# Kernel optimization log

Measured on AMD Instinct MI355X. Metric: run time of the kernel, lower is better.

The kernel has to match this reference:

```python
import jax, jax.numpy as jnp
import numpy as np

N_NODES = 20000  # number of batch nodes (static for segment ops)

def setup_inputs() -> dict:
    key = jax.random.key(0)
    N, E, V, D = N_NODES, 640000, 100000, 64
    ks = jax.random.split(key, 8)
    nodes = jax.random.randint(ks[0], (N,), 0, V)
    neigh_idx = jax.random.randint(ks[1], (E,), 0, V)
    seg_ids = jnp.sort(jax.random.randint(ks[2], (E,), 0, N))  # ragged degrees, sorted by node
    u2e = jax.random.normal(ks[3], (V, D), jnp.float32) * 0.02
    s1 = 1.0 / np.sqrt(2 * D)
    s2 = 1.0 / np.sqrt(D)
    att1_w = jax.random.uniform(ks[4], (2 * D, D), jnp.float32, -s1, s1)
    att1_b = jnp.zeros((D,), jnp.float32)
    att2_w = jax.random.uniform(ks[5], (D, D), jnp.float32, -s2, s2)
    att2_b = jnp.zeros((D,), jnp.float32)
    att3_w = jax.random.uniform(ks[6], (D, 1), jnp.float32, -s2, s2)
    att3_b = jnp.zeros((1,), jnp.float32)
    return dict(nodes=nodes, neigh_idx=neigh_idx, seg_ids=seg_ids, u2e=u2e,
                att1_w=att1_w, att1_b=att1_b, att2_w=att2_w, att2_b=att2_b,
                att3_w=att3_w, att3_b=att3_b)


def reference(nodes, neigh_idx, seg_ids, u2e, att1_w, att1_b, att2_w, att2_b, att3_w, att3_b):
    # Ragged per-node neighbor attention, flattened over all edges.
    e_u = u2e[neigh_idx]              # [E, D] neighbor embeddings
    u_rep = u2e[nodes][seg_ids]       # [E, D] center-node embedding broadcast per edge
    x = jnp.concatenate([e_u, u_rep], axis=1)            # [E, 2D]
    x = jax.nn.relu(x @ att1_w + att1_b)                  # [E, D]
    x = jax.nn.relu(x @ att2_w + att2_b)                  # [E, D]
    logits = (x @ att3_w + att3_b)[:, 0]                  # [E]
    # segment softmax over each node's neighbor set
    m = jax.ops.segment_max(logits, seg_ids, num_segments=N_NODES)
    m = jnp.where(jnp.isfinite(m), m, 0.0)                # guard empty segments
    ex = jnp.exp(logits - m[seg_ids])
    denom = jax.ops.segment_sum(ex, seg_ids, num_segments=N_NODES)
    att = ex / jnp.maximum(denom[seg_ids], 1e-9)          # [E]
    # attention-weighted sum of neighbor embeddings per node (e_u^T @ att_w per node)
    out = jax.ops.segment_sum(att[:, None] * e_u, seg_ids, num_segments=N_NODES)  # [N, D]
    return out
```

## Files before the change

### kernel.cpp

```cpp
#include <hip/hip_runtime.h>
#include <hip/hip_bf16.h>

typedef __attribute__((ext_vector_type(8))) short bf16x8;
typedef __attribute__((ext_vector_type(4))) float f32x4;

__device__ __forceinline__ unsigned short f2bf(float f) {
    unsigned x = __float_as_uint(f);
    unsigned r = (x + 0x7FFF + ((x >> 16) & 1)) >> 16;
    return (unsigned short)r;
}
__device__ __forceinline__ bf16x8 cvt8(const float* __restrict__ p) {
    bf16x8 r;
#pragma unroll
    for (int j = 0; j < 8; ++j) r[j] = (short)f2bf(p[j]);
    return r;
}
__device__ __forceinline__ unsigned pack_relu_bf16(unsigned yv, unsigned zv) {
    float lo = fmaxf(__uint_as_float(yv << 16) + __uint_as_float(zv << 16), 0.0f);
    float hi = fmaxf(__uint_as_float(yv & 0xFFFF0000u) + __uint_as_float(zv & 0xFFFF0000u), 0.0f);
    __hip_bfloat162 p = __float22bfloat162_rn(float2{lo, hi});
    return *(unsigned*)&p;
}

template <bool BF>
__launch_bounds__(256)
__global__ void conv_all_k(const float* __restrict__ u2e,
                           const int* __restrict__ nodes,
                           const int* __restrict__ segs,
                           const float* __restrict__ w1,
                           const float* __restrict__ w2,
                           const float* __restrict__ b1f,
                           unsigned short* __restrict__ u2ebf,
                           unsigned short* __restrict__ Y,
                           unsigned short* __restrict__ z,
                           unsigned short* __restrict__ w2t,
                           int* __restrict__ seg_off,
                           int V, int N, int E, int yb, int zb) {
    __shared__ __align__(16) unsigned short w1l[64 * 136];
    const int bid = blockIdx.x;
    const int t = threadIdx.x;
    const int wid = t >> 6;
    const int lane = t & 63;
    const int q = lane >> 4;
    const int m15 = lane & 15;

    if (bid < yb + zb) {
        for (int i = t; i < 128 * 64; i += 256) {
            int k = i >> 6, n = i & 63;
            w1l[n * 136 + k] = f2bf(w1[i]);
        }
        __syncthreads();

        if (bid < yb) {
            const int wbase = (bid * 4 + wid) * 16;
            if (wbase >= V) return;
            int row = min(wbase + m15, V - 1);
            const float* p = u2e + (long)row * 64;
            bf16x8 a0 = cvt8(p + q * 8);
            bf16x8 a1 = cvt8(p + 32 + q * 8);
            if (BF && wbase + m15 < V) {
                *(bf16x8*)(u2ebf + (long)row * 64 + q * 8) = a0;
                *(bf16x8*)(u2ebf + (long)row * 64 + 32 + q * 8) = a1;
            }
            f32x4 acc[4];
#pragma unroll
            for (int b = 0; b < 4; ++b) {
                acc[b] = (f32x4){0.f, 0.f, 0.f, 0.f};
                const unsigned short* wr = w1l + (b * 16 + m15) * 136;
                acc[b] = __builtin_amdgcn_mfma_f32_16x16x32_bf16(
                    a0, *(const bf16x8*)(wr + q * 8), acc[b], 0, 0, 0);
                acc[b] = __builtin_amdgcn_mfma_f32_16x16x32_bf16(
                    a1, *(const bf16x8*)(wr + 32 + q * 8), acc[b], 0, 0, 0);
            }
#pragma unroll
            for (int b = 0; b < 4; ++b)
#pragma unroll
                for (int r = 0; r < 4; ++r) {
                    int rr = wbase + q * 4 + r;
                    if (rr < V) Y[(long)rr * 64 + b * 16 + m15] = f2bf(acc[b][r]);
                }
        } else {
            const int wbase = ((bid - yb) * 4 + wid) * 16;
            if (wbase >= N) return;
            int nd = nodes[min(wbase + m15, N - 1)];
            const float* p = u2e + (long)nd * 64;
            bf16x8 a0 = cvt8(p + q * 8);
            bf16x8 a1 = cvt8(p + 32 + q * 8);
            f32x4 acc[4];
#pragma unroll
            for (int b = 0; b < 4; ++b) {
                float bv = b1f[b * 16 + m15];
                acc[b] = (f32x4){bv, bv, bv, bv};
                const unsigned short* wr = w1l + (b * 16 + m15) * 136;
                acc[b] = __builtin_amdgcn_mfma_f32_16x16x32_bf16(
                    a0, *(const bf16x8*)(wr + 64 + q * 8), acc[b], 0, 0, 0);
                acc[b] = __builtin_amdgcn_mfma_f32_16x16x32_bf16(
                    a1, *(const bf16x8*)(wr + 96 + q * 8), acc[b], 0, 0, 0);
            }
#pragma unroll
            for (int b = 0; b < 4; ++b)
#pragma unroll
                for (int r = 0; r < 4; ++r) {
                    int rr = wbase + q * 4 + r;
                    if (rr < N) z[(long)rr * 64 + b * 16 + m15] = f2bf(acc[b][r]);
                }
        }
    } else if (bid == yb + zb) {
        for (int i = t; i < 64 * 64; i += 256) {
            int k = i >> 6, n = i & 63;
            w2t[n * 64 + k] = f2bf(w2[i]);
        }
    } else {
        int idx = (bid - yb - zb - 1) * 256 + t;
        if (idx > N) return;
        int l = 0, r = E;
        while (l < r) { int mid = (l + r) >> 1; if (segs[mid] < idx) l = mid + 1; else r = mid; }
        seg_off[idx] = l;
    }
}

__launch_bounds__(256)
__global__ void logits2_k(const int* __restrict__ neigh,
                          const int* __restrict__ segs,
                          const unsigned short* __restrict__ Y,
                          const unsigned short* __restrict__ z,
                          const unsigned short* __restrict__ w2t,
                          const float* __restrict__ b2f,
                          const float* __restrict__ w3f, const float* __restrict__ b3f,
                          float* __restrict__ ex, int E) {
    const int wid = threadIdx.x >> 6;
    const int lane = threadIdx.x & 63;
    const int q = lane >> 4;
    const int m15 = lane & 15;
    const long base = ((long)blockIdx.x * 4 + wid) * 32;
    if (base >= E) return;

    int vi[2], sg[2];
#pragma unroll
    for (int g = 0; g < 2; ++g) {
        long e = base + g * 16 + m15;
        int ec = (int)(e < E ? e : (long)E - 1);
        vi[g] = neigh[ec];
        sg[g] = segs[ec];
    }
    bf16x8 y0[2], y1[2], zz0[2], zz1[2];
#pragma unroll
    for (int g = 0; g < 2; ++g) {
        const unsigned short* yr = Y + (long)vi[g] * 64;
        y0[g] = *(const bf16x8*)(yr + q * 8);
        y1[g] = *(const bf16x8*)(yr + 32 + q * 8);
        const unsigned short* zr = z + (long)sg[g] * 64;
        zz0[g] = *(const bf16x8*)(zr + q * 8);
        zz1[g] = *(const bf16x8*)(zr + 32 + q * 8);
    }

    f32x4 acc[2][4];
#pragma unroll
    for (int g = 0; g < 2; ++g) {
        bf16x8 h0, h1;
#pragma unroll
        for (int j = 0; j < 4; ++j) {
            ((unsigned*)&h0)[j] = pack_relu_bf16(((unsigned*)&y0[g])[j], ((unsigned*)&zz0[g])[j]);
            ((unsigned*)&h1)[j] = pack_relu_bf16(((unsigned*)&y1[g])[j], ((unsigned*)&zz1[g])[j]);
        }
#pragma unroll
        for (int b = 0; b < 4; ++b) {
            float bv = b2f[b * 16 + m15];
            acc[g][b] = (f32x4){bv, bv, bv, bv};
            const bf16x8* wrow = (const bf16x8*)(w2t + (b * 16 + m15) * 64);
            acc[g][b] = __builtin_amdgcn_mfma_f32_16x16x32_bf16(h0, wrow[0 + q], acc[g][b], 0, 0, 0);
            acc[g][b] = __builtin_amdgcn_mfma_f32_16x16x32_bf16(h1, wrow[4 + q], acc[g][b], 0, 0, 0);
        }
    }

    const float b3v = b3f[0];
#pragma unroll
    for (int g = 0; g < 2; ++g)
#pragma unroll
        for (int r = 0; r < 4; ++r) {
            float v = 0.0f;
#pragma unroll
            for (int b = 0; b < 4; ++b) v += fmaxf(acc[g][b][r], 0.0f) * w3f[b * 16 + m15];
            v += __shfl_xor(v, 1);
            v += __shfl_xor(v, 2);
            v += __shfl_xor(v, 4);
            v += __shfl_xor(v, 8);
            long ee = base + g * 16 + q * 4 + r;
            if (m15 == r && ee < E) ex[ee] = __expf(v + b3v);
        }
}

template <bool BF>
__launch_bounds__(256)
__global__ void aggw_k(const int* __restrict__ seg_off,
                       const int* __restrict__ neigh,
                       const unsigned short* __restrict__ u2ebf,
                       const float* __restrict__ u2e,
                       const float* __restrict__ ex,
                       float* __restrict__ out, int N) {
    const int wid = threadIdx.x >> 6;
    const int lane = threadIdx.x & 63;
    const int n = blockIdx.x * 4 + wid;
    if (n >= N) return;
    const int lo = seg_off[n];
    const int hi = seg_off[n + 1];
    const int slot = lane >> 3;
    const int cl = lane & 7;

    float a[8] = {0.f, 0.f, 0.f, 0.f, 0.f, 0.f, 0.f, 0.f};
    float s = 0.0f;

    for (int e = lo + slot; e < hi; e += 8) {
        float w = ex[e];
        int vi = neigh[e];
        s += w;
        if constexpr (BF) {
            bf16x8 v = *(const bf16x8*)(u2ebf + (long)vi * 64 + cl * 8);
            const unsigned* vd = (const unsigned*)&v;
#pragma unroll
            for (int j = 0; j < 4; ++j) {
                a[2 * j]     = fmaf(w, __uint_as_float(vd[j] << 16), a[2 * j]);
                a[2 * j + 1] = fmaf(w, __uint_as_float(vd[j] & 0xFFFF0000u), a[2 * j + 1]);
            }
        } else {
            const float* row = u2e + (long)vi * 64 + cl * 8;
            float4 v0 = *(const float4*)row;
            float4 v1 = *(const float4*)(row + 4);
            a[0] = fmaf(w, v0.x, a[0]); a[1] = fmaf(w, v0.y, a[1]);
            a[2] = fmaf(w, v0.z, a[2]); a[3] = fmaf(w, v0.w, a[3]);
            a[4] = fmaf(w, v1.x, a[4]); a[5] = fmaf(w, v1.y, a[5]);
            a[6] = fmaf(w, v1.z, a[6]); a[7] = fmaf(w, v1.w, a[7]);
        }
    }
#pragma unroll
    for (int msk = 8; msk <= 32; msk <<= 1) {
        s += __shfl_xor(s, msk);
#pragma unroll
        for (int j = 0; j < 8; ++j) a[j] += __shfl_xor(a[j], msk);
    }
    if (slot == 0) {
        float inv = 1.0f / fmaxf(s, 1e-9f);
        float4 o0 = {a[0] * inv, a[1] * inv, a[2] * inv, a[3] * inv};
        float4 o1 = {a[4] * inv, a[5] * inv, a[6] * inv, a[7] * inv};
        float* op = out + (long)n * 64 + cl * 8;
        *(float4*)op = o0;
        *(float4*)(op + 4) = o1;
    }
}

__global__ void prep_bounds_k(const float* __restrict__ w1,
                              const float* __restrict__ w2,
                              const int* __restrict__ segs,
                              unsigned short* __restrict__ w1t,
                              unsigned short* __restrict__ w2t,
                              int* __restrict__ seg_off, int N, int E) {
    int t = threadIdx.x;
    if (blockIdx.x == 0) {
        for (int i = t; i < 128 * 64; i += 256) {
            int k = i >> 6, n = i & 63;
            w1t[n * 128 + k] = f2bf(w1[i]);
        }
        for (int i = t; i < 64 * 64; i += 256) {
            int k = i >> 6, n = i & 63;
            w2t[n * 64 + k] = f2bf(w2[i]);
        }
    } else {
        int idx = (blockIdx.x - 1) * 256 + t;
        if (idx > N) return;
        int l = 0, r = E;
        while (l < r) { int mid = (l + r) >> 1; if (segs[mid] < idx) l = mid + 1; else r = mid; }
        seg_off[idx] = l;
    }
}

__launch_bounds__(256)
__global__ void logits_fb_k(const int* __restrict__ nodes,
                            const int* __restrict__ neigh,
                            const int* __restrict__ segs,
                            const float* __restrict__ u2e,
                            const unsigned short* __restrict__ w1t,
                            const unsigned short* __restrict__ w2t,
                            const float* __restrict__ b1f, const float* __restrict__ b2f,
                            const float* __restrict__ w3f, const float* __restrict__ b3f,
                            float* __restrict__ ex, int E) {
    __shared__ __align__(16) unsigned short h1buf[4][16 * 72];
    const int wid = threadIdx.x >> 6;
    const int lane = threadIdx.x & 63;
    const int q = lane >> 4;
    const int m15 = lane & 15;
    const long base = ((long)blockIdx.x * 4 + wid) * 16;
    long ee0 = base + m15;
    int e = (int)(ee0 < E ? ee0 : (long)E - 1);
    int ni = neigh[e];
    int ctr = nodes[segs[e]];
    const float* eu = u2e + (long)ni * 64;
    const float* ur = u2e + (long)ctr * 64;
    bf16x8 a0 = cvt8(eu + q * 8), a1 = cvt8(eu + 32 + q * 8);
    bf16x8 a2 = cvt8(ur + q * 8), a3 = cvt8(ur + 32 + q * 8);
    f32x4 acc[4];
#pragma unroll
    for (int b = 0; b < 4; ++b) {
        float bvv = b1f[b * 16 + m15];
        acc[b] = (f32x4){bvv, bvv, bvv, bvv};
        const bf16x8* wrow = (const bf16x8*)(w1t + (b * 16 + m15) * 128);
        acc[b] = __builtin_amdgcn_mfma_f32_16x16x32_bf16(a0, wrow[0 + q], acc[b], 0, 0, 0);
        acc[b] = __builtin_amdgcn_mfma_f32_16x16x32_bf16(a1, wrow[4 + q], acc[b], 0, 0, 0);
        acc[b] = __builtin_amdgcn_mfma_f32_16x16x32_bf16(a2, wrow[8 + q], acc[b], 0, 0, 0);
        acc[b] = __builtin_amdgcn_mfma_f32_16x16x32_bf16(a3, wrow[12 + q], acc[b], 0, 0, 0);
    }
#pragma unroll
    for (int b = 0; b < 4; ++b)
#pragma unroll
        for (int r = 0; r < 4; ++r)
            h1buf[wid][(q * 4 + r) * 72 + b * 16 + m15] = f2bf(fmaxf(acc[b][r], 0.0f));
    const unsigned short* hrow = &h1buf[wid][m15 * 72];
    bf16x8 h0 = *(const bf16x8*)(hrow + q * 8);
    bf16x8 h1 = *(const bf16x8*)(hrow + 32 + q * 8);
    f32x4 acc2[4];
#pragma unroll
    for (int b = 0; b < 4; ++b) {
        float bvv = b2f[b * 16 + m15];
        acc2[b] = (f32x4){bvv, bvv, bvv, bvv};
        const bf16x8* wrow = (const bf16x8*)(w2t + (b * 16 + m15) * 64);
        acc2[b] = __builtin_amdgcn_mfma_f32_16x16x32_bf16(h0, wrow[0 + q], acc2[b], 0, 0, 0);
        acc2[b] = __builtin_amdgcn_mfma_f32_16x16x32_bf16(h1, wrow[4 + q], acc2[b], 0, 0, 0);
    }
    float b3v = b3f[0];
#pragma unroll
    for (int r = 0; r < 4; ++r) {
        float v = 0.0f;
#pragma unroll
        for (int b = 0; b < 4; ++b) v += fmaxf(acc2[b][r], 0.0f) * w3f[b * 16 + m15];
        v += __shfl_xor(v, 1);
        v += __shfl_xor(v, 2);
        v += __shfl_xor(v, 4);
        v += __shfl_xor(v, 8);
        long ee = base + q * 4 + r;
        if (m15 == r && ee < E) ex[ee] = __expf(v + b3v);
    }
}

extern "C" void kernel_launch(void* const* d_in, const int* in_sizes, int n_in,
                              void* d_out, int out_size, void* d_ws, size_t ws_size,
                              hipStream_t stream) {
    const int* nodes = (const int*)d_in[0];
    const int* neigh = (const int*)d_in[1];
    const int* segs  = (const int*)d_in[2];
    const float* u2e = (const float*)d_in[3];
    const float* w1  = (const float*)d_in[4];
    const float* b1  = (const float*)d_in[5];
    const float* w2  = (const float*)d_in[6];
    const float* b2  = (const float*)d_in[7];
    const float* w3  = (const float*)d_in[8];
    const float* b3  = (const float*)d_in[9];
    const int N = in_sizes[0];
    const int E = in_sizes[1];
    const long VD = in_sizes[3];
    const int V = (int)(VD / 64);

    char* ws = (char*)d_ws;
    size_t off = 0;
    auto alloc = [&](size_t bytes) { char* p = ws + off; off = (off + bytes + 255) & ~(size_t)255; return p; };
    float* ex = (float*)alloc((size_t)E * 4);
    int* seg_off = (int*)alloc((size_t)(N + 1) * 4);
    unsigned short* w1t = (unsigned short*)alloc(128 * 64 * 2);
    unsigned short* w2t = (unsigned short*)alloc(64 * 64 * 2);
    size_t need_min = off;
    unsigned short* Y = (unsigned short*)alloc((size_t)VD * 2);
    unsigned short* zb = (unsigned short*)alloc((size_t)N * 64 * 2);
    size_t need_t2 = off;
    unsigned short* u2ebf = (unsigned short*)alloc((size_t)VD * 2);
    size_t need_t1 = off;
    (void)need_min;

    float* out = (float*)d_out;

    const int yb = ((V + 15) / 16 + 3) / 4;
    const int zbk = ((N + 15) / 16 + 3) / 4;
    const int bblocks = (N + 256) / 256;
    const int lblocks = ((E + 31) / 32 + 3) / 4;
    const int ablocks = (N + 3) / 4;

    if (ws_size >= need_t1) {
        conv_all_k<true><<<yb + zbk + 1 + bblocks, 256, 0, stream>>>(
            u2e, nodes, segs, w1, w2, b1, u2ebf, Y, zb, w2t, seg_off, V, N, E, yb, zbk);
        logits2_k<<<lblocks, 256, 0, stream>>>(neigh, segs, Y, zb, w2t, b2, w3, b3, ex, E);
        aggw_k<true><<<ablocks, 256, 0, stream>>>(seg_off, neigh, u2ebf, nullptr, ex, out, N);
    } else if (ws_size >= need_t2) {
        conv_all_k<false><<<yb + zbk + 1 + bblocks, 256, 0, stream>>>(
            u2e, nodes, segs, w1, w2, b1, nullptr, Y, zb, w2t, seg_off, V, N, E, yb, zbk);
        logits2_k<<<lblocks, 256, 0, stream>>>(neigh, segs, Y, zb, w2t, b2, w3, b3, ex, E);
        aggw_k<false><<<ablocks, 256, 0, stream>>>(seg_off, neigh, nullptr, u2e, ex, out, N);
    } else {
        const int pbblocks = 1 + (N + 256) / 256;
        prep_bounds_k<<<pbblocks, 256, 0, stream>>>(w1, w2, segs, w1t, w2t, seg_off, N, E);
        const int blocks1 = ((E + 15) / 16 + 3) / 4;
        logits_fb_k<<<blocks1, 256, 0, stream>>>(nodes, neigh, segs, u2e, w1t, w2t,
                                                 b1, b2, w3, b3, ex, E);
        aggw_k<false><<<ablocks, 256, 0, stream>>>(seg_off, neigh, nullptr, u2e, ex, out, N);
    }
}
```

Baseline: 154.7 us.

## Make conv kernel persistent and cache only the needed half of W1

Measured after the change: 152.1 us. Within noise of the previous version (-1.7%).

```diff
diff --git a/kernel.cpp b/kernel.cpp
--- a/kernel.cpp
+++ b/kernel.cpp
@@ -35,8 +35,9 @@
                            unsigned short* __restrict__ z,
                            unsigned short* __restrict__ w2t,
                            int* __restrict__ seg_off,
-                           int V, int N, int E, int yb, int zb) {
-    __shared__ __align__(16) unsigned short w1l[64 * 136];
+                           int V, int N, int E, int yblk, int zblk,
+                           int ytiles, int ztiles) {
+    __shared__ __align__(16) unsigned short w1l[64 * 72];
     const int bid = blockIdx.x;
     const int t = threadIdx.x;
     const int wid = t >> 6;
@@ -44,74 +45,89 @@
     const int q = lane >> 4;
     const int m15 = lane & 15;
 
-    if (bid < yb + zb) {
-        for (int i = t; i < 128 * 64; i += 256) {
-            int k = i >> 6, n = i & 63;
-            w1l[n * 136 + k] = f2bf(w1[i]);
+    if (bid < yblk + zblk) {
+        const bool isY = bid < yblk;
+        const int kbase = isY ? 0 : 64;
+        for (int u = t; u < 64 * 16; u += 256) {
+            int k = u >> 4;
+            int n4 = (u & 15) * 4;
+            float4 v = *(const float4*)(w1 + (long)(kbase + k) * 64 + n4);
+            w1l[(n4 + 0) * 72 + k] = f2bf(v.x);
+            w1l[(n4 + 1) * 72 + k] = f2bf(v.y);
+            w1l[(n4 + 2) * 72 + k] = f2bf(v.z);
+            w1l[(n4 + 3) * 72 + k] = f2bf(v.w);
         }
         __syncthreads();
 
-        if (bid < yb) {
-            const int wbase = (bid * 4 + wid) * 16;
-            if (wbase >= V) return;
-            int row = min(wbase + m15, V - 1);
-            const float* p = u2e + (long)row * 64;
-            bf16x8 a0 = cvt8(p + q * 8);
-            bf16x8 a1 = cvt8(p + 32 + q * 8);
-            if (BF && wbase + m15 < V) {
-                *(bf16x8*)(u2ebf + (long)row * 64 + q * 8) = a0;
-                *(bf16x8*)(u2ebf + (long)row * 64 + 32 + q * 8) = a1;
+        bf16x8 wb0[4], wb1[4];
+#pragma unroll
+        for (int b = 0; b < 4; ++b) {
+            const unsigned short* wr = w1l + (b * 16 + m15) * 72;
+            wb0[b] = *(const bf16x8*)(wr + q * 8);
+            wb1[b] = *(const bf16x8*)(wr + 32 + q * 8);
+        }
+
+        if (isY) {
+            for (int tile = bid; tile < ytiles; tile += yblk) {
+                const int wbase = tile * 64 + wid * 16;
+                if (wbase >= V) continue;
+                int row = min(wbase + m15, V - 1);
+                const float* p = u2e + (long)row * 64;
+                bf16x8 a0 = cvt8(p + q * 8);
+                bf16x8 a1 = cvt8(p + 32 + q * 8);
+                if (BF && wbase + m15 < V) {
+                    *(bf16x8*)(u2ebf + (long)row * 64 + q * 8) = a0;
+                    *(bf16x8*)(u2ebf + (long)row * 64 + 32 + q * 8) = a1;
+                }
+                f32x4 acc[4];
+#pragma unroll
+                for (int b = 0; b < 4; ++b) {
+                    acc[b] = (f32x4){0.f, 0.f, 0.f, 0.f};
+                    acc[b] = __builtin_amdgcn_mfma_f32_16x16x32_bf16(a0, wb0[b], acc[b], 0, 0, 0);
+                    acc[b] = __builtin_amdgcn_mfma_f32_16x16x32_bf16(a1, wb1[b], acc[b], 0, 0, 0);
+                }
+#pragma unroll
+                for (int b = 0; b < 4; ++b)
+#pragma unroll
+                    for (int r = 0; r < 4; ++r) {
+                        int rr = wbase + q * 4 + r;
+                        if (rr < V) Y[(long)rr * 64 + b * 16 + m15] = f2bf(acc[b][r]);
+                    }
             }
-            f32x4 acc[4];
-#pragma unroll
-            for (int b = 0; b < 4; ++b) {
-                acc[b] = (f32x4){0.f, 0.f, 0.f, 0.f};
-                const unsigned short* wr = w1l + (b * 16 + m15) * 136;
-                acc[b] = __builtin_amdgcn_mfma_f32_16x16x32_bf16(
-                    a0, *(const bf16x8*)(wr + q * 8), acc[b], 0, 0, 0);
-                acc[b] = __builtin_amdgcn_mfma_f32_16x16x32_bf16(
-                    a1, *(const bf16x8*)(wr + 32 + q * 8), acc[b], 0, 0, 0);
+        } else {
+            float b1v[4];
+#pragma unroll
+            for (int b = 0; b < 4; ++b) b1v[b] = b1f[b * 16 + m15];
+            for (int tile = bid - yblk; tile < ztiles; tile += zblk) {
+                const int wbase = tile * 64 + wid * 16;
+                if (wbase >= N) continue;
+                int nd = nodes[min(wbase + m15, N - 1)];
+                const float* p = u2e + (long)nd * 64;
+                bf16x8 a0 = cvt8(p + q * 8);
+                bf16x8 a1 = cvt8(p + 32 + q * 8);
+                f32x4 acc[4];
+#pragma unroll
+                for (int b = 0; b < 4; ++b) {
+                    acc[b] = (f32x4){b1v[b], b1v[b], b1v[b], b1v[b]};
+                    acc[b] = __builtin_amdgcn_mfma_f32_16x16x32_bf16(a0, wb0[b], acc[b], 0, 0, 0);
+                    acc[b] = __builtin_amdgcn_mfma_f32_16x16x32_bf16(a1, wb1[b], acc[b], 0, 0, 0);
+                }
+#pragma unroll
+                for (int b = 0; b < 4; ++b)
+#pragma unroll
+                    for (int r = 0; r < 4; ++r) {
+                        int rr = wbase + q * 4 + r;
+                        if (rr < N) z[(long)rr * 64 + b * 16 + m15] = f2bf(acc[b][r]);
+                    }
             }
-#pragma unroll
-            for (int b = 0; b < 4; ++b)
-#pragma unroll
-                for (int r = 0; r < 4; ++r) {
-                    int rr = wbase + q * 4 + r;
-                    if (rr < V) Y[(long)rr * 64 + b * 16 + m15] = f2bf(acc[b][r]);
-                }
-        } else {
-            const int wbase = ((bid - yb) * 4 + wid) * 16;
-            if (wbase >= N) return;
-            int nd = nodes[min(wbase + m15, N - 1)];
-            const float* p = u2e + (long)nd * 64;
-            bf16x8 a0 = cvt8(p + q * 8);
-            bf16x8 a1 = cvt8(p + 32 + q * 8);
-            f32x4 acc[4];
-#pragma unroll
-            for (int b = 0; b < 4; ++b) {
-                float bv = b1f[b * 16 + m15];
-                acc[b] = (f32x4){bv, bv, bv, bv};
-                const unsigned short* wr = w1l + (b * 16 + m15) * 136;
-                acc[b] = __builtin_amdgcn_mfma_f32_16x16x32_bf16(
-                    a0, *(const bf16x8*)(wr + 64 + q * 8), acc[b], 0, 0, 0);
-                acc[b] = __builtin_amdgcn_mfma_f32_16x16x32_bf16(
-                    a1, *(const bf16x8*)(wr + 96 + q * 8), acc[b], 0, 0, 0);
-            }
-#pragma unroll
-            for (int b = 0; b < 4; ++b)
-#pragma unroll
-                for (int r = 0; r < 4; ++r) {
-                    int rr = wbase + q * 4 + r;
-                    if (rr < N) z[(long)rr * 64 + b * 16 + m15] = f2bf(acc[b][r]);
-                }
-        }
-    } else if (bid == yb + zb) {
+        }
+    } else if (bid == yblk + zblk) {
         for (int i = t; i < 64 * 64; i += 256) {
             int k = i >> 6, n = i & 63;
             w2t[n * 64 + k] = f2bf(w2[i]);
         }
     } else {
-        int idx = (bid - yb - zb - 1) * 256 + t;
+        int idx = (bid - yblk - zblk - 1) * 256 + t;
         if (idx > N) return;
         int l = 0, r = E;
         while (l < r) { int mid = (l + r) >> 1; if (segs[mid] < idx) l = mid + 1; else r = mid; }
@@ -154,6 +170,13 @@
         zz1[g] = *(const bf16x8*)(zr + 32 + q * 8);
     }
 
+    float b2v[4], w3v[4];
+#pragma unroll
+    for (int b = 0; b < 4; ++b) {
+        b2v[b] = b2f[b * 16 + m15];
+        w3v[b] = w3f[b * 16 + m15];
+    }
+
     f32x4 acc[2][4];
 #pragma unroll
     for (int g = 0; g < 2; ++g) {
@@ -165,8 +188,7 @@
         }
 #pragma unroll
         for (int b = 0; b < 4; ++b) {
-            float bv = b2f[b * 16 + m15];
-            acc[g][b] = (f32x4){bv, bv, bv, bv};
+            acc[g][b] = (f32x4){b2v[b], b2v[b], b2v[b], b2v[b]};
             const bf16x8* wrow = (const bf16x8*)(w2t + (b * 16 + m15) * 64);
             acc[g][b] = __builtin_amdgcn_mfma_f32_16x16x32_bf16(h0, wrow[0 + q], acc[g][b], 0, 0, 0);
             acc[g][b] = __builtin_amdgcn_mfma_f32_16x16x32_bf16(h1, wrow[4 + q], acc[g][b], 0, 0, 0);
@@ -180,7 +202,7 @@
         for (int r = 0; r < 4; ++r) {
             float v = 0.0f;
 #pragma unroll
-            for (int b = 0; b < 4; ++b) v += fmaxf(acc[g][b][r], 0.0f) * w3f[b * 16 + m15];
+            for (int b = 0; b < 4; ++b) v += fmaxf(acc[g][b][r], 0.0f) * w3v[b];
             v += __shfl_xor(v, 1);
             v += __shfl_xor(v, 2);
             v += __shfl_xor(v, 4);
@@ -375,20 +397,24 @@
 
     float* out = (float*)d_out;
 
-    const int yb = ((V + 15) / 16 + 3) / 4;
-    const int zbk = ((N + 15) / 16 + 3) / 4;
+    const int ytiles = (V + 63) / 64;
+    const int ztiles = (N + 63) / 64;
+    const int yblk = ytiles < 640 ? ytiles : 640;
+    const int zblk = ztiles < 160 ? ztiles : 160;
     const int bblocks = (N + 256) / 256;
     const int lblocks = ((E + 31) / 32 + 3) / 4;
     const int ablocks = (N + 3) / 4;
 
     if (ws_size >= need_t1) {
-        conv_all_k<true><<<yb + zbk + 1 + bblocks, 256, 0, stream>>>(
-            u2e, nodes, segs, w1, w2, b1, u2ebf, Y, zb, w2t, seg_off, V, N, E, yb, zbk);
+        conv_all_k<true><<<yblk + zblk + 1 + bblocks, 256, 0, stream>>>(
+            u2e, nodes, segs, w1, w2, b1, u2ebf, Y, zb, w2t, seg_off, V, N, E,
+            yblk, zblk, ytiles, ztiles);
         logits2_k<<<lblocks, 256, 0, stream>>>(neigh, segs, Y, zb, w2t, b2, w3, b3, ex, E);
         aggw_k<true><<<ablocks, 256, 0, stream>>>(seg_off, neigh, u2ebf, nullptr, ex, out, N);
     } else if (ws_size >= need_t2) {
-        conv_all_k<false><<<yb + zbk + 1 + bblocks, 256, 0, stream>>>(
-            u2e, nodes, segs, w1, w2, b1, nullptr, Y, zb, w2t, seg_off, V, N, E, yb, zbk);
+        conv_all_k<false><<<yblk + zblk + 1 + bblocks, 256, 0, stream>>>(
+            u2e, nodes, segs, w1, w2, b1, nullptr, Y, zb, w2t, seg_off, V, N, E,
+            yblk, zblk, ytiles, ztiles);
         logits2_k<<<lblocks, 256, 0, stream>>>(neigh, segs, Y, zb, w2t, b2, w3, b3, ex, E);
         aggw_k<false><<<ablocks, 256, 0, stream>>>(seg_off, neigh, nullptr, u2e, ex, out, N);
     } else {
```

## Fuse MLP, softmax numerator and aggregation into one per-edge kernel with atomics

Applied to the files above, without the earlier changes.

Measured after the change: 237.2 us. 1.53x slower.

```diff
diff --git a/kernel.cpp b/kernel.cpp
--- a/kernel.cpp
+++ b/kernel.cpp
@@ -10,242 +10,159 @@
     return (unsigned short)r;
 }
 __device__ __forceinline__ bf16x8 cvt8(const float* __restrict__ p) {
+    float4 v0 = *(const float4*)p;
+    float4 v1 = *(const float4*)(p + 4);
     bf16x8 r;
-#pragma unroll
-    for (int j = 0; j < 8; ++j) r[j] = (short)f2bf(p[j]);
+    r[0] = (short)f2bf(v0.x); r[1] = (short)f2bf(v0.y);
+    r[2] = (short)f2bf(v0.z); r[3] = (short)f2bf(v0.w);
+    r[4] = (short)f2bf(v1.x); r[5] = (short)f2bf(v1.y);
+    r[6] = (short)f2bf(v1.z); r[7] = (short)f2bf(v1.w);
     return r;
 }
-__device__ __forceinline__ unsigned pack_relu_bf16(unsigned yv, unsigned zv) {
-    float lo = fmaxf(__uint_as_float(yv << 16) + __uint_as_float(zv << 16), 0.0f);
-    float hi = fmaxf(__uint_as_float(yv & 0xFFFF0000u) + __uint_as_float(zv & 0xFFFF0000u), 0.0f);
-    __hip_bfloat162 p = __float22bfloat162_rn(float2{lo, hi});
-    return *(unsigned*)&p;
-}
-
-template <bool BF>
-__launch_bounds__(256)
-__global__ void conv_all_k(const float* __restrict__ u2e,
-                           const int* __restrict__ nodes,
-                           const int* __restrict__ segs,
-                           const float* __restrict__ w1,
-                           const float* __restrict__ w2,
-                           const float* __restrict__ b1f,
-                           unsigned short* __restrict__ u2ebf,
-                           unsigned short* __restrict__ Y,
-                           unsigned short* __restrict__ z,
-                           unsigned short* __restrict__ w2t,
-                           int* __restrict__ seg_off,
-                           int V, int N, int E, int yb, int zb) {
-    __shared__ __align__(16) unsigned short w1l[64 * 136];
+
+__launch_bounds__(256)
+__global__ void prep_f_k(const float* __restrict__ w1,
+                         const float* __restrict__ w2,
+                         unsigned short* __restrict__ w1t,
+                         unsigned short* __restrict__ w2t,
+                         float* __restrict__ zout,
+                         float* __restrict__ den, int N) {
     const int bid = blockIdx.x;
     const int t = threadIdx.x;
-    const int wid = t >> 6;
-    const int lane = t & 63;
-    const int q = lane >> 4;
-    const int m15 = lane & 15;
-
-    if (bid < yb + zb) {
+    if (bid == 0) {
         for (int i = t; i < 128 * 64; i += 256) {
             int k = i >> 6, n = i & 63;
-            w1l[n * 136 + k] = f2bf(w1[i]);
-        }
-        __syncthreads();
-
-        if (bid < yb) {
-            const int wbase = (bid * 4 + wid) * 16;
-            if (wbase >= V) return;
-            int row = min(wbase + m15, V - 1);
-            const float* p = u2e + (long)row * 64;
-            bf16x8 a0 = cvt8(p + q * 8);
-            bf16x8 a1 = cvt8(p + 32 + q * 8);
-            if (BF && wbase + m15 < V) {
-                *(bf16x8*)(u2ebf + (long)row * 64 + q * 8) = a0;
-                *(bf16x8*)(u2ebf + (long)row * 64 + 32 + q * 8) = a1;
-            }
-            f32x4 acc[4];
-#pragma unroll
-            for (int b = 0; b < 4; ++b) {
-                acc[b] = (f32x4){0.f, 0.f, 0.f, 0.f};
-                const unsigned short* wr = w1l + (b * 16 + m15) * 136;
-                acc[b] = __builtin_amdgcn_mfma_f32_16x16x32_bf16(
-                    a0, *(const bf16x8*)(wr + q * 8), acc[b], 0, 0, 0);
-                acc[b] = __builtin_amdgcn_mfma_f32_16x16x32_bf16(
-                    a1, *(const bf16x8*)(wr + 32 + q * 8), acc[b], 0, 0, 0);
-            }
-#pragma unroll
-            for (int b = 0; b < 4; ++b)
-#pragma unroll
-                for (int r = 0; r < 4; ++r) {
-                    int rr = wbase + q * 4 + r;
-                    if (rr < V) Y[(long)rr * 64 + b * 16 + m15] = f2bf(acc[b][r]);
-                }
-        } else {
-            const int wbase = ((bid - yb) * 4 + wid) * 16;
-            if (wbase >= N) return;
-            int nd = nodes[min(wbase + m15, N - 1)];
-            const float* p = u2e + (long)nd * 64;
-            bf16x8 a0 = cvt8(p + q * 8);
-            bf16x8 a1 = cvt8(p + 32 + q * 8);
-            f32x4 acc[4];
-#pragma unroll
-            for (int b = 0; b < 4; ++b) {
-                float bv = b1f[b * 16 + m15];
-                acc[b] = (f32x4){bv, bv, bv, bv};
-                const unsigned short* wr = w1l + (b * 16 + m15) * 136;
-                acc[b] = __builtin_amdgcn_mfma_f32_16x16x32_bf16(
-                    a0, *(const bf16x8*)(wr + 64 + q * 8), acc[b], 0, 0, 0);
-                acc[b] = __builtin_amdgcn_mfma_f32_16x16x32_bf16(
-                    a1, *(const bf16x8*)(wr + 96 + q * 8), acc[b], 0, 0, 0);
-            }
-#pragma unroll
-            for (int b = 0; b < 4; ++b)
-#pragma unroll
-                for (int r = 0; r < 4; ++r) {
-                    int rr = wbase + q * 4 + r;
-                    if (rr < N) z[(long)rr * 64 + b * 16 + m15] = f2bf(acc[b][r]);
-                }
-        }
-    } else if (bid == yb + zb) {
+            w1t[n * 128 + k] = f2bf(w1[i]);
+        }
+    } else if (bid == 1) {
         for (int i = t; i < 64 * 64; i += 256) {
             int k = i >> 6, n = i & 63;
             w2t[n * 64 + k] = f2bf(w2[i]);
         }
     } else {
-        int idx = (bid - yb - zb - 1) * 256 + t;
-        if (idx > N) return;
-        int l = 0, r = E;
-        while (l < r) { int mid = (l + r) >> 1; if (segs[mid] < idx) l = mid + 1; else r = mid; }
-        seg_off[idx] = l;
-    }
-}
-
-__launch_bounds__(256)
-__global__ void logits2_k(const int* __restrict__ neigh,
-                          const int* __restrict__ segs,
-                          const unsigned short* __restrict__ Y,
-                          const unsigned short* __restrict__ z,
-                          const unsigned short* __restrict__ w2t,
-                          const float* __restrict__ b2f,
-                          const float* __restrict__ w3f, const float* __restrict__ b3f,
-                          float* __restrict__ ex, int E) {
+        long zt = (long)(bid - 2) * 256 + t;
+        long nth = (long)(gridDim.x - 2) * 256;
+        f32x4 zz = (f32x4){0.f, 0.f, 0.f, 0.f};
+        for (long i = zt; i < (long)N * 16; i += nth) ((f32x4*)zout)[i] = zz;
+        for (long i = zt; i < (long)((N + 3) / 4); i += nth) ((f32x4*)den)[i] = zz;
+    }
+}
+
+__launch_bounds__(256)
+__global__ void fused_all_k(const int* __restrict__ nodes,
+                            const int* __restrict__ neigh,
+                            const int* __restrict__ segs,
+                            const float* __restrict__ u2e,
+                            const unsigned short* __restrict__ w1t,
+                            const unsigned short* __restrict__ w2t,
+                            const float* __restrict__ b1f,
+                            const float* __restrict__ b2f,
+                            const float* __restrict__ w3f,
+                            const float* __restrict__ b3f,
+                            float* __restrict__ outp,
+                            float* __restrict__ den, int E) {
+    __shared__ __align__(16) unsigned short h1buf[4][16 * 72];
     const int wid = threadIdx.x >> 6;
     const int lane = threadIdx.x & 63;
     const int q = lane >> 4;
     const int m15 = lane & 15;
-    const long base = ((long)blockIdx.x * 4 + wid) * 32;
+    const long base = ((long)blockIdx.x * 4 + wid) * 16;
     if (base >= E) return;
 
-    int vi[2], sg[2];
-#pragma unroll
-    for (int g = 0; g < 2; ++g) {
-        long e = base + g * 16 + m15;
-        int ec = (int)(e < E ? e : (long)E - 1);
-        vi[g] = neigh[ec];
-        sg[g] = segs[ec];
-    }
-    bf16x8 y0[2], y1[2], zz0[2], zz1[2];
-#pragma unroll
-    for (int g = 0; g < 2; ++g) {
-        const unsigned short* yr = Y + (long)vi[g] * 64;
-        y0[g] = *(const bf16x8*)(yr + q * 8);
-        y1[g] = *(const bf16x8*)(yr + 32 + q * 8);
-        const unsigned short* zr = z + (long)sg[g] * 64;
-        zz0[g] = *(const bf16x8*)(zr + q * 8);
-        zz1[g] = *(const bf16x8*)(zr + 32 + q * 8);
-    }
-
-    f32x4 acc[2][4];
-#pragma unroll
-    for (int g = 0; g < 2; ++g) {
-        bf16x8 h0, h1;
-#pragma unroll
-        for (int j = 0; j < 4; ++j) {
-            ((unsigned*)&h0)[j] = pack_relu_bf16(((unsigned*)&y0[g])[j], ((unsigned*)&zz0[g])[j]);
-            ((unsigned*)&h1)[j] = pack_relu_bf16(((unsigned*)&y1[g])[j], ((unsigned*)&zz1[g])[j]);
-        }
-#pragma unroll
-        for (int b = 0; b < 4; ++b) {
-            float bv = b2f[b * 16 + m15];
-            acc[g][b] = (f32x4){bv, bv, bv, bv};
-            const bf16x8* wrow = (const bf16x8*)(w2t + (b * 16 + m15) * 64);
-            acc[g][b] = __builtin_amdgcn_mfma_f32_16x16x32_bf16(h0, wrow[0 + q], acc[g][b], 0, 0, 0);
-            acc[g][b] = __builtin_amdgcn_mfma_f32_16x16x32_bf16(h1, wrow[4 + q], acc[g][b], 0, 0, 0);
-        }
-    }
-
+    long ee0 = base + m15;
+    int ec = (int)(ee0 < E ? ee0 : (long)E - 1);
+    int vi = neigh[ec];
+    int sg = segs[ec];
+    int ctr = nodes[sg];
+
+    float uvv[16];
+#pragma unroll
+    for (int j = 0; j < 16; ++j) {
+        int svi = __builtin_amdgcn_readlane(vi, j);
+        uvv[j] = u2e[((long)svi << 6) + lane];
+    }
+
+    const float* eu = u2e + (long)vi * 64;
+    const float* ur = u2e + (long)ctr * 64;
+    bf16x8 a0 = cvt8(eu + q * 8), a1 = cvt8(eu + 32 + q * 8);
+    bf16x8 a2 = cvt8(ur + q * 8), a3 = cvt8(ur + 32 + q * 8);
+
+    f32x4 acc[4];
+#pragma unroll
+    for (int b = 0; b < 4; ++b) {
+        float bvv = b1f[b * 16 + m15];
+        acc[b] = (f32x4){bvv, bvv, bvv, bvv};
+        const bf16x8* wrow = (const bf16x8*)(w1t + (b * 16 + m15) * 128);
+        acc[b] = __builtin_amdgcn_mfma_f32_16x16x32_bf16(a0, wrow[0 + q], acc[b], 0, 0, 0);
+        acc[b] = __builtin_amdgcn_mfma_f32_16x16x32_bf16(a1, wrow[4 + q], acc[b], 0, 0, 0);
+        acc[b] = __builtin_amdgcn_mfma_f32_16x16x32_bf16(a2, wrow[8 + q], acc[b], 0, 0, 0);
+        acc[b] = __builtin_amdgcn_mfma_f32_16x16x32_bf16(a3, wrow[12 + q], acc[b], 0, 0, 0);
+    }
+#pragma unroll
+    for (int b = 0; b < 4; ++b)
+#pragma unroll
+        for (int r = 0; r < 4; ++r)
+            h1buf[wid][(q * 4 + r) * 72 + b * 16 + m15] = f2bf(fmaxf(acc[b][r], 0.0f));
+    const unsigned short* hrow = &h1buf[wid][m15 * 72];
+    bf16x8 h0 = *(const bf16x8*)(hrow + q * 8);
+    bf16x8 h1 = *(const bf16x8*)(hrow + 32 + q * 8);
+
+    f32x4 acc2[4];
+#pragma unroll
+    for (int b = 0; b < 4; ++b) {
+        float bvv = b2f[b * 16 + m15];
+        acc2[b] = (f32x4){bvv, bvv, bvv, bvv};
+        const bf16x8* wrow = (const bf16x8*)(w2t + (b * 16 + m15) * 64);
+        acc2[b] = __builtin_amdgcn_mfma_f32_16x16x32_bf16(h0, wrow[0 + q], acc2[b], 0, 0, 0);
+        acc2[b] = __builtin_amdgcn_mfma_f32_16x16x32_bf16(h1, wrow[4 + q], acc2[b], 0, 0, 0);
+    }
     const float b3v = b3f[0];
-#pragma unroll
-    for (int g = 0; g < 2; ++g)
-#pragma unroll
-        for (int r = 0; r < 4; ++r) {
-            float v = 0.0f;
-#pragma unroll
-            for (int b = 0; b < 4; ++b) v += fmaxf(acc[g][b][r], 0.0f) * w3f[b * 16 + m15];
-            v += __shfl_xor(v, 1);
-            v += __shfl_xor(v, 2);
-            v += __shfl_xor(v, 4);
-            v += __shfl_xor(v, 8);
-            long ee = base + g * 16 + q * 4 + r;
-            if (m15 == r && ee < E) ex[ee] = __expf(v + b3v);
-        }
-}
-
-template <bool BF>
-__launch_bounds__(256)
-__global__ void aggw_k(const int* __restrict__ seg_off,
-                       const int* __restrict__ neigh,
-                       const unsigned short* __restrict__ u2ebf,
-                       const float* __restrict__ u2e,
-                       const float* __restrict__ ex,
-                       float* __restrict__ out, int N) {
-    const int wid = threadIdx.x >> 6;
-    const int lane = threadIdx.x & 63;
-    const int n = blockIdx.x * 4 + wid;
-    if (n >= N) return;
-    const int lo = seg_off[n];
-    const int hi = seg_off[n + 1];
-    const int slot = lane >> 3;
-    const int cl = lane & 7;
-
-    float a[8] = {0.f, 0.f, 0.f, 0.f, 0.f, 0.f, 0.f, 0.f};
-    float s = 0.0f;
-
-    for (int e = lo + slot; e < hi; e += 8) {
-        float w = ex[e];
-        int vi = neigh[e];
-        s += w;
-        if constexpr (BF) {
-            bf16x8 v = *(const bf16x8*)(u2ebf + (long)vi * 64 + cl * 8);
-            const unsigned* vd = (const unsigned*)&v;
-#pragma unroll
-            for (int j = 0; j < 4; ++j) {
-                a[2 * j]     = fmaf(w, __uint_as_float(vd[j] << 16), a[2 * j]);
-                a[2 * j + 1] = fmaf(w, __uint_as_float(vd[j] & 0xFFFF0000u), a[2 * j + 1]);
-            }
-        } else {
-            const float* row = u2e + (long)vi * 64 + cl * 8;
-            float4 v0 = *(const float4*)row;
-            float4 v1 = *(const float4*)(row + 4);
-            a[0] = fmaf(w, v0.x, a[0]); a[1] = fmaf(w, v0.y, a[1]);
-            a[2] = fmaf(w, v0.z, a[2]); a[3] = fmaf(w, v0.w, a[3]);
-            a[4] = fmaf(w, v1.x, a[4]); a[5] = fmaf(w, v1.y, a[5]);
-            a[6] = fmaf(w, v1.z, a[6]); a[7] = fmaf(w, v1.w, a[7]);
-        }
-    }
-#pragma unroll
-    for (int msk = 8; msk <= 32; msk <<= 1) {
-        s += __shfl_xor(s, msk);
-#pragma unroll
-        for (int j = 0; j < 8; ++j) a[j] += __shfl_xor(a[j], msk);
-    }
-    if (slot == 0) {
-        float inv = 1.0f / fmaxf(s, 1e-9f);
-        float4 o0 = {a[0] * inv, a[1] * inv, a[2] * inv, a[3] * inv};
-        float4 o1 = {a[4] * inv, a[5] * inv, a[6] * inv, a[7] * inv};
-        float* op = out + (long)n * 64 + cl * 8;
-        *(float4*)op = o0;
-        *(float4*)(op + 4) = o1;
-    }
+    float ev[4];
+#pragma unroll
+    for (int r = 0; r < 4; ++r) {
+        float v = 0.0f;
+#pragma unroll
+        for (int b = 0; b < 4; ++b) v += fmaxf(acc2[b][r], 0.0f) * w3f[b * 16 + m15];
+        v += __shfl_xor(v, 1);
+        v += __shfl_xor(v, 2);
+        v += __shfl_xor(v, 4);
+        v += __shfl_xor(v, 8);
+        ev[r] = __expf(v + b3v);
+    }
+    int rsel = m15 & 3;
+    float exval = rsel == 0 ? ev[0] : (rsel == 1 ? ev[1] : (rsel == 2 ? ev[2] : ev[3]));
+    float exm = __shfl(exval, ((m15 >> 2) << 4) | (m15 & 3));
+    if (base + m15 >= E) exm = 0.0f;
+
+    float a = 0.0f;
+    float ds = 0.0f;
+    int cur = __builtin_amdgcn_readlane(sg, 0);
+#pragma unroll
+    for (int j = 0; j < 16; ++j) {
+        int ssg = __builtin_amdgcn_readlane(sg, j);
+        float sex = __uint_as_float(
+            (unsigned)__builtin_amdgcn_readlane(__float_as_uint(exm), j));
+        if (ssg != cur) {
+            atomicAdd(outp + (long)cur * 64 + lane, a);
+            if (lane == 0) atomicAdd(den + cur, ds);
+            a = 0.0f; ds = 0.0f; cur = ssg;
+        }
+        a = fmaf(sex, uvv[j], a);
+        ds += sex;
+    }
+    atomicAdd(outp + (long)cur * 64 + lane, a);
+    if (lane == 0) atomicAdd(den + cur, ds);
+}
+
+__launch_bounds__(256)
+__global__ void div_k(float* __restrict__ out, const float* __restrict__ den, int N) {
+    int i = blockIdx.x * 256 + threadIdx.x;
+    if (i >= N * 16) return;
+    float inv = 1.0f / fmaxf(den[i >> 4], 1e-9f);
+    f32x4* p = (f32x4*)out + i;
+    f32x4 v = *p;
+    v[0] *= inv; v[1] *= inv; v[2] *= inv; v[3] *= inv;
+    *p = v;
 }
 
 __global__ void prep_bounds_k(const float* __restrict__ w1,
@@ -340,6 +257,52 @@
     }
 }
 
+__launch_bounds__(256)
+__global__ void aggw_f32_k(const int* __restrict__ seg_off,
+                           const int* __restrict__ neigh,
+                           const float* __restrict__ u2e,
+                           const float* __restrict__ ex,
+                           float* __restrict__ out, int N) {
+    const int wid = threadIdx.x >> 6;
+    const int lane = threadIdx.x & 63;
+    const int n = blockIdx.x * 4 + wid;
+    if (n >= N) return;
+    const int lo = seg_off[n];
+    const int hi = seg_off[n + 1];
+    const int slot = lane >> 3;
+    const int cl = lane & 7;
+
+    float a[8] = {0.f, 0.f, 0.f, 0.f, 0.f, 0.f, 0.f, 0.f};
+    float s = 0.0f;
+
+    for (int e = lo + slot; e < hi; e += 8) {
+        float w = ex[e];
+        int vi = neigh[e];
+        s += w;
+        const float* row = u2e + (long)vi * 64 + cl * 8;
+        float4 v0 = *(const float4*)row;
+        float4 v1 = *(const float4*)(row + 4);
+        a[0] = fmaf(w, v0.x, a[0]); a[1] = fmaf(w, v0.y, a[1]);
+        a[2] = fmaf(w, v0.z, a[2]); a[3] = fmaf(w, v0.w, a[3]);
+        a[4] = fmaf(w, v1.x, a[4]); a[5] = fmaf(w, v1.y, a[5]);
+        a[6] = fmaf(w, v1.z, a[6]); a[7] = fmaf(w, v1.w, a[7]);
+    }
+#pragma unroll
+    for (int msk = 8; msk <= 32; msk <<= 1) {
+        s += __shfl_xor(s, msk);
+#pragma unroll
+        for (int j = 0; j < 8; ++j) a[j] += __shfl_xor(a[j], msk);
+    }
+    if (slot == 0) {
+        float inv = 1.0f / fmaxf(s, 1e-9f);
+        float4 o0 = {a[0] * inv, a[1] * inv, a[2] * inv, a[3] * inv};
+        float4 o1 = {a[4] * inv, a[5] * inv, a[6] * inv, a[7] * inv};
+        float* op = out + (long)n * 64 + cl * 8;
+        *(float4*)op = o0;
+        *(float4*)(op + 4) = o1;
+    }
+}
+
 extern "C" void kernel_launch(void* const* d_in, const int* in_sizes, int n_in,
                               void* d_out, int out_size, void* d_ws, size_t ws_size,
                               hipStream_t stream) {
@@ -355,8 +318,6 @@
     const float* b3  = (const float*)d_in[9];
     const int N = in_sizes[0];
     const int E = in_sizes[1];
-    const long VD = in_sizes[3];
-    const int V = (int)(VD / 64);
 
     char* ws = (char*)d_ws;
     size_t off = 0;
@@ -365,38 +326,25 @@
     int* seg_off = (int*)alloc((size_t)(N + 1) * 4);
     unsigned short* w1t = (unsigned short*)alloc(128 * 64 * 2);
     unsigned short* w2t = (unsigned short*)alloc(64 * 64 * 2);
-    size_t need_min = off;
-    unsigned short* Y = (unsigned short*)alloc((size_t)VD * 2);
-    unsigned short* zb = (unsigned short*)alloc((size_t)N * 64 * 2);
-    size_t need_t2 = off;
-    unsigned short* u2ebf = (unsigned short*)alloc((size_t)VD * 2);
-    size_t need_t1 = off;
-    (void)need_min;
+    size_t need_t3 = off;
+    float* den = (float*)alloc((size_t)N * 4);
+    size_t need_f = off;
 
     float* out = (float*)d_out;
 
-    const int yb = ((V + 15) / 16 + 3) / 4;
-    const int zbk = ((N + 15) / 16 + 3) / 4;
-    const int bblocks = (N + 256) / 256;
-    const int lblocks = ((E + 31) / 32 + 3) / 4;
+    const int fblocks = ((E + 15) / 16 + 3) / 4;
     const int ablocks = (N + 3) / 4;
 
-    if (ws_size >= need_t1) {
-        conv_all_k<true><<<yb + zbk + 1 + bblocks, 256, 0, stream>>>(
-            u2e, nodes, segs, w1, w2, b1, u2ebf, Y, zb, w2t, seg_off, V, N, E, yb, zbk);
-        logits2_k<<<lblocks, 256, 0, stream>>>(neigh, segs, Y, zb, w2t, b2, w3, b3, ex, E);
-        aggw_k<true><<<ablocks, 256, 0, stream>>>(seg_off, neigh, u2ebf, nullptr, ex, out, N);
-    } else if (ws_size >= need_t2) {
-        conv_all_k<false><<<yb + zbk + 1 + bblocks, 256, 0, stream>>>(
-            u2e, nodes, segs, w1, w2, b1, nullptr, Y, zb, w2t, seg_off, V, N, E, yb, zbk);
-        logits2_k<<<lblocks, 256, 0, stream>>>(neigh, segs, Y, zb, w2t, b2, w3, b3, ex, E);
-        aggw_k<false><<<ablocks, 256, 0, stream>>>(seg_off, neigh, nullptr, u2e, ex, out, N);
+    if (ws_size >= need_f) {
+        prep_f_k<<<128, 256, 0, stream>>>(w1, w2, w1t, w2t, out, den, N);
+        fused_all_k<<<fblocks, 256, 0, stream>>>(
+            nodes, neigh, segs, u2e, w1t, w2t, b1, b2, w3, b3, out, den, E);
+        div_k<<<(N * 16 + 255) / 256, 256, 0, stream>>>(out, den, N);
     } else {
         const int pbblocks = 1 + (N + 256) / 256;
         prep_bounds_k<<<pbblocks, 256, 0, stream>>>(w1, w2, segs, w1t, w2t, seg_off, N, E);
-        const int blocks1 = ((E + 15) / 16 + 3) / 4;
-        logits_fb_k<<<blocks1, 256, 0, stream>>>(nodes, neigh, segs, u2e, w1t, w2t,
+        logits_fb_k<<<fblocks, 256, 0, stream>>>(nodes, neigh, segs, u2e, w1t, w2t,
                                                  b1, b2, w3, b3, ex, E);
-        aggw_k<false><<<ablocks, 256, 0, stream>>>(seg_off, neigh, nullptr, u2e, ex, out, N);
-    }
-}
+        aggw_f32_k<<<ablocks, 256, 0, stream>>>(seg_off, neigh, u2e, ex, out, N);
+    }
+}
```
